# Performance work log

Hardware: AMD Instinct MI355X
Metric: run time of the kernel (lower is better)

The kernel has to match this reference:

```python
import jax, jax.numpy as jnp
import numpy as np

N_NODES = 100000
N_EDGES = 1600000
N_GRAPHS = 128
IN_CH, OUT_CH, N_CLASS = 768, 128, 2


def setup_inputs() -> dict:
    key = jax.random.key(0)
    ks = jax.random.split(key, 8)
    x = jax.random.normal(ks[0], (N_NODES, IN_CH), dtype=jnp.float32)
    # directed edges with src < dst so to_undirected (concat + reverse) has no duplicates
    src = jax.random.randint(ks[1], (N_EDGES,), 0, N_NODES - 1, dtype=jnp.int32)
    dst = jax.random.randint(ks[2], (N_EDGES,), 1, N_NODES, dtype=jnp.int32)
    dst = jnp.where(dst <= src, src + 1, dst)  # ensure src < dst (no self-loops)
    edge_index = jnp.stack([src, dst], axis=0)
    batch = jnp.sort(jax.random.randint(ks[3], (N_NODES,), 0, N_GRAPHS, dtype=jnp.int32))
    s = 0.05
    return {
        "x": x,
        "edge_index": edge_index,
        "batch": batch,
        "num_graphs": N_GRAPHS,
        "W_conv": jax.random.normal(ks[4], (IN_CH, OUT_CH), dtype=jnp.float32) * s,
        "b_conv": jnp.zeros((OUT_CH,), dtype=jnp.float32),
        "W_lin0": jax.random.normal(ks[5], (IN_CH, OUT_CH), dtype=jnp.float32) * s,
        "b_lin0": jnp.zeros((OUT_CH,), dtype=jnp.float32),
        "W_lin1": jax.random.normal(ks[6], (2 * OUT_CH, OUT_CH), dtype=jnp.float32) * s,
        "b_lin1": jnp.zeros((OUT_CH,), dtype=jnp.float32),
        "W_lin2": jax.random.normal(ks[7], (OUT_CH, N_CLASS), dtype=jnp.float32) * s,
        "b_lin2": jnp.zeros((N_CLASS,), dtype=jnp.float32),
    }


def _gcn_conv(x, W, b, src, dst, n_nodes):
    # GCNConv: linear transform, add self-loops, symmetric normalization, scatter-add
    loop = jnp.arange(n_nodes, dtype=src.dtype)
    s = jnp.concatenate([src, loop])
    d = jnp.concatenate([dst, loop])
    deg = jax.ops.segment_sum(jnp.ones_like(d, dtype=x.dtype), d, num_segments=n_nodes)
    dinv = jnp.where(deg > 0, jax.lax.rsqrt(deg), 0.0)
    norm = dinv[s] * dinv[d]  # [E']
    h = x @ W  # [N, out]
    msg = h[s] * norm[:, None]  # gather + scale
    return jax.ops.segment_sum(msg, d, num_segments=n_nodes) + b


def reference(x, edge_index, batch, num_graphs, W_conv, b_conv,
              W_lin0, b_lin0, W_lin1, b_lin1, W_lin2, b_lin2):
    n_nodes = x.shape[0]
    # to_undirected: add reversed edges (input has src<dst so no duplicates to coalesce)
    src = jnp.concatenate([edge_index[0], edge_index[1]])
    dst = jnp.concatenate([edge_index[1], edge_index[0]])
    h = jax.nn.relu(_gcn_conv(x, W_conv, b_conv, src, dst, n_nodes))
    # global max pool over graphs
    h = jax.ops.segment_max(h, batch, num_segments=num_graphs)  # [G, out]
    # root node = first node of each graph (batch is sorted)
    root = jax.ops.segment_min(jnp.arange(n_nodes), batch, num_segments=num_graphs)
    news = jax.nn.relu(x[root] @ W_lin0 + b_lin0)  # [G, out]
    h = jax.nn.relu(jnp.concatenate([news, h], axis=-1) @ W_lin1 + b_lin1)
    logits = h @ W_lin2 + b_lin2
    return jax.nn.log_softmax(logits, axis=-1)
```

## Files before the change

### kernel.cpp

```cpp
#include <hip/hip_runtime.h>

#define N_NODES 100000
#define N_EDGES 1600000
#define N_GRAPHS 128
#define IN_CH 768
#define OUT_CH 128

#define BSHIFT 8
#define NBKT ((N_NODES + 255) / 256)
#define EPB 8000
#define CAPREC 16384
#define PADV 16
#define CAPADJ (CAPREC + 256 * (PADV - 1))

using short8 = __attribute__((ext_vector_type(8))) short;
using f32x4  = __attribute__((ext_vector_type(4))) float;

__device__ __forceinline__ float bf2f(unsigned short u) {
    return __uint_as_float(((unsigned)u) << 16);
}
__device__ __forceinline__ unsigned short f2bf(float f) {
    unsigned u = __float_as_uint(f);
    u += 0x7fffu + ((u >> 16) & 1u);
    return (unsigned short)(u >> 16);
}
__device__ __forceinline__ float load_f(const void* p, size_t i, int f32) {
    return f32 ? ((const float*)p)[i] : bf2f(((const unsigned short*)p)[i]);
}
__device__ __forceinline__ float lo16(unsigned p) { return __uint_as_float(p << 16); }
__device__ __forceinline__ float hi16(unsigned p) { return __uint_as_float(p & 0xffff0000u); }

__global__ void k_init(int* flag, int* gcur, unsigned* pooled, int* root,
                       const int* __restrict__ batch, const unsigned short* __restrict__ xbits,
                       const void* Wc, const void* bc, const void* W0, const void* b0,
                       const void* W1, const void* b1, const void* W2, const void* b2,
                       unsigned short* Wt, float* fbc, float* fW0, float* fb0,
                       float* fW1, float* fb1, float* fW2, float* fb2) {
    __shared__ int sflag;
    if (threadIdx.x == 0) sflag = 0;
    __syncthreads();
    int bad = 0;
    for (int j = threadIdx.x; j < 8192; j += 256) {
        float v = bf2f(xbits[j]);
        if (!(v > -64.f && v < 64.f)) bad = 1;
    }
    if (bad) atomicOr(&sflag, 1);
    __syncthreads();
    int f32 = sflag;
    int i = blockIdx.x * blockDim.x + threadIdx.x;
    if (i == 0) *flag = f32;
    if (i < NBKT) gcur[i] = i * CAPREC;
    if (i < N_GRAPHS * OUT_CH) pooled[i] = 0u;
    if (i < N_NODES) {
        int b = batch[i];
        if (i == 0 || batch[i - 1] != b) root[b] = i;
    }
    if (i < IN_CH * OUT_CH) {
        int n = i / IN_CH, k = i - n * IN_CH;
        Wt[i] = f32 ? f2bf(((const float*)Wc)[k * OUT_CH + n])
                    : ((const unsigned short*)Wc)[k * OUT_CH + n];
        fW0[i] = load_f(W0, i, f32);
    }
    if (i < 2 * OUT_CH * OUT_CH) fW1[i] = load_f(W1, i, f32);
    if (i < OUT_CH * 2) fW2[i] = load_f(W2, i, f32);
    if (i < OUT_CH) { fbc[i] = load_f(bc, i, f32); fb0[i] = load_f(b0, i, f32); fb1[i] = load_f(b1, i, f32); }
    if (i < 2) fb2[i] = load_f(b2, i, f32);
}

__global__ __launch_bounds__(256) void k_bin(const int* __restrict__ src, const int* __restrict__ dst,
                                             int* gcur, unsigned* __restrict__ binned) {
    __shared__ int hist[NBKT];
    __shared__ int basep[NBKT];
    int t = threadIdx.x;
    for (int b = t; b < NBKT; b += 256) hist[b] = 0;
    __syncthreads();
    int e0 = blockIdx.x * EPB, e1 = e0 + EPB;
    if (e1 > N_EDGES) e1 = N_EDGES;
    for (int i = e0 + t; i < e1; i += 256) {
        unsigned s_ = (unsigned)src[i]; if (s_ >= N_NODES) s_ = N_NODES - 1u;
        unsigned d_ = (unsigned)dst[i]; if (d_ >= N_NODES) d_ = N_NODES - 1u;
        atomicAdd(&hist[d_ >> BSHIFT], 1);
        atomicAdd(&hist[s_ >> BSHIFT], 1);
    }
    __syncthreads();
    for (int b = t; b < NBKT; b += 256) {
        int c = hist[b];
        if (c) {
            int base = atomicAdd(&gcur[b], c);
            basep[b] = (base + c <= (b + 1) * CAPREC) ? base : -1;
        }
        hist[b] = 0;
    }
    __syncthreads();
    for (int i = e0 + t; i < e1; i += 256) {
        unsigned s_ = (unsigned)src[i]; if (s_ >= N_NODES) s_ = N_NODES - 1u;
        unsigned d_ = (unsigned)dst[i]; if (d_ >= N_NODES) d_ = N_NODES - 1u;
        unsigned bd = d_ >> BSHIFT, bs = s_ >> BSHIFT;
        int pd_ = basep[bd], ps_ = basep[bs];
        int od = atomicAdd(&hist[bd], 1);
        int os = atomicAdd(&hist[bs], 1);
        if (pd_ >= 0) binned[pd_ + od] = (s_ << 8) | (d_ & 255u);
        if (ps_ >= 0) binned[ps_ + os] = (d_ << 8) | (s_ & 255u);
    }
}

__global__ __launch_bounds__(256) void k_build(const unsigned* __restrict__ binned,
                                               const int* __restrict__ gcur,
                                               int2* odeg, float* dinv, int* adj) {
    __shared__ int sdeg[256], scur[256], sscan[256];
    int b = blockIdx.x, t = threadIdx.x;
    int base = b * CAPREC;
    int n = gcur[b] - base;
    if (n > CAPREC) n = CAPREC;
    if (n < 0) n = 0;
    int base_adj = b * CAPADJ;
    sdeg[t] = 0;
    __syncthreads();
    for (int j = t; j < n; j += 256) atomicAdd(&sdeg[binned[base + j] & 255u], 1);
    __syncthreads();
    int myd = sdeg[t];
    int pd = (myd + PADV - 1) & ~(PADV - 1);
    sscan[t] = pd;
    __syncthreads();
    for (int off = 1; off < 256; off <<= 1) {
        int add = (t >= off) ? sscan[t - off] : 0;
        __syncthreads();
        sscan[t] += add;
        __syncthreads();
    }
    int excl = sscan[t] - pd;
    int node = (b << BSHIFT) + t;
    if (node < N_NODES) {
        odeg[node] = make_int2(base_adj + excl, pd);
        dinv[node] = rsqrtf((float)(myd + 1));
    }
    for (int j = myd; j < pd; j++) adj[base_adj + excl + j] = N_NODES;
    scur[t] = excl;
    __syncthreads();
    for (int j = t; j < n; j += 256) {
        unsigned rec = binned[base + j];
        int loc = rec & 255u;
        adj[base_adj + atomicAdd(&scur[loc], 1)] = (int)(rec >> 8);
    }
}

#define MBLK 128
#define BK 64
#define LSTR 72

__global__ __launch_bounds__(256) void k_gemm(const int* __restrict__ flag,
                                              const void* __restrict__ xv,
                                              const unsigned short* __restrict__ Wt,
                                              const float* __restrict__ dinv,
                                              unsigned short* __restrict__ h) {
    __shared__ __align__(16) unsigned short As[MBLK * LSTR];
    __shared__ __align__(16) unsigned short Bs[OUT_CH * LSTR];
    const int f32 = *flag;
    const int tid = threadIdx.x;
    if (blockIdx.x == 0 && tid < 64) ((unsigned*)(h + (size_t)N_NODES * OUT_CH))[tid] = 0u;
    const int wave = tid >> 6, lane = tid & 63;
    const int quad = lane >> 4, l16 = lane & 15;
    const int wm = (wave >> 1) * 64, wn = (wave & 1) * 64;
    const int row0 = blockIdx.x * MBLK;

    f32x4 acc[4][4];
#pragma unroll
    for (int mt = 0; mt < 4; mt++)
#pragma unroll
        for (int nt = 0; nt < 4; nt++) acc[mt][nt] = (f32x4){0.f, 0.f, 0.f, 0.f};

    int r_[4], c8_[4];
    size_t arow_[4];
#pragma unroll
    for (int i = 0; i < 4; i++) {
        int chunk = tid + i * 256;
        r_[i] = chunk >> 3;
        c8_[i] = (chunk & 7) << 3;
        int gr = row0 + r_[i]; if (gr >= N_NODES) gr = N_NODES - 1;
        arow_[i] = (size_t)gr * IN_CH;
    }

    float4 fa[4][2];
    uint4  ua[4];
    uint4  rb[4];

#define LOADK(K0)                                                                      \
    {                                                                                  \
        if (f32) {                                                                     \
            _Pragma("unroll") for (int i = 0; i < 4; i++) {                            \
                const float* xp = (const float*)xv + arow_[i] + (K0) + c8_[i];         \
                fa[i][0] = *(const float4*)xp;                                         \
                fa[i][1] = *(const float4*)(xp + 4);                                   \
            }                                                                          \
        } else {                                                                       \
            _Pragma("unroll") for (int i = 0; i < 4; i++)                              \
                ua[i] = *(const uint4*)((const unsigned short*)xv + arow_[i] + (K0) + c8_[i]); \
        }                                                                              \
        _Pragma("unroll") for (int i = 0; i < 4; i++)                                  \
            rb[i] = *(const uint4*)(Wt + (size_t)r_[i] * IN_CH + (K0) + c8_[i]);       \
    }

#define STOREK()                                                                       \
    {                                                                                  \
        if (f32) {                                                                     \
            _Pragma("unroll") for (int i = 0; i < 4; i++) {                            \
                uint4 va;                                                              \
                va.x = (unsigned)f2bf(fa[i][0].x) | ((unsigned)f2bf(fa[i][0].y) << 16);\
                va.y = (unsigned)f2bf(fa[i][0].z) | ((unsigned)f2bf(fa[i][0].w) << 16);\
                va.z = (unsigned)f2bf(fa[i][1].x) | ((unsigned)f2bf(fa[i][1].y) << 16);\
                va.w = (unsigned)f2bf(fa[i][1].z) | ((unsigned)f2bf(fa[i][1].w) << 16);\
                *(uint4*)&As[r_[i] * LSTR + c8_[i]] = va;                              \
                *(uint4*)&Bs[r_[i] * LSTR + c8_[i]] = rb[i];                           \
            }                                                                          \
        } else {                                                                       \
            _Pragma("unroll") for (int i = 0; i < 4; i++) {                            \
                *(uint4*)&As[r_[i] * LSTR + c8_[i]] = ua[i];                           \
                *(uint4*)&Bs[r_[i] * LSTR + c8_[i]] = rb[i];                           \
            }                                                                          \
        }                                                                              \
    }

#define COMPUTE()                                                                      \
    {                                                                                  \
        _Pragma("unroll") for (int kk = 0; kk < BK; kk += 32) {                        \
            short8 af[4], bf[4];                                                       \
            _Pragma("unroll") for (int mt = 0; mt < 4; mt++)                           \
                af[mt] = *(const short8*)&As[(wm + mt * 16 + l16) * LSTR + kk + quad * 8]; \
            _Pragma("unroll") for (int nt = 0; nt < 4; nt++)                           \
                bf[nt] = *(const short8*)&Bs[(wn + nt * 16 + l16) * LSTR + kk + quad * 8]; \
            _Pragma("unroll") for (int mt = 0; mt < 4; mt++)                           \
                _Pragma("unroll") for (int nt = 0; nt < 4; nt++)                       \
                    acc[mt][nt] = __builtin_amdgcn_mfma_f32_16x16x32_bf16(af[mt], bf[nt], acc[mt][nt], 0, 0, 0); \
        }                                                                              \
    }

    LOADK(0);
    STOREK();
    __syncthreads();
    for (int k0 = BK;; k0 += BK) {
        bool more = (k0 < IN_CH);
        if (more) LOADK(k0);
        COMPUTE();
        if (!more) break;
        __syncthreads();
        STOREK();
        __syncthreads();
    }

#pragma unroll
    for (int mt = 0; mt < 4; mt++) {
#pragma unroll
        for (int r = 0; r < 4; r++) {
            int m = row0 + wm + mt * 16 + quad * 4 + r;
            if (m >= N_NODES) continue;
            float dvm = dinv[m];
#pragma unroll
            for (int nt = 0; nt < 4; nt++) {
                int col = wn + nt * 16 + l16;
                h[(size_t)m * OUT_CH + col] = f2bf(acc[mt][nt][r] * dvm);
            }
        }
    }
#undef LOADK
#undef STOREK
#undef COMPUTE
}

__global__ __launch_bounds__(256) void k_agg(const unsigned short* __restrict__ h,
                                             const int* __restrict__ adj,
                                             const int2* __restrict__ odeg,
                                             const float* __restrict__ dinv,
                                             const int* __restrict__ batch,
                                             const float* __restrict__ fbc,
                                             unsigned* pooled) {
    int wave = threadIdx.x >> 6, lane = threadIdx.x & 63;
    int node = blockIdx.x * 4 + wave;
    float dv = dinv[node];
    int l16 = lane & 15;

    uint4 own = *(const uint4*)(h + (size_t)node * OUT_CH + l16 * 8);
    float gsel = (lane < 16) ? 1.f : 0.f;
    float a0 = lo16(own.x) * gsel, a1 = hi16(own.x) * gsel;
    float a2 = lo16(own.y) * gsel, a3 = hi16(own.y) * gsel;
    float a4 = lo16(own.z) * gsel, a5 = hi16(own.z) * gsel;
    float a6 = lo16(own.w) * gsel, a7 = hi16(own.w) * gsel;

    int2 od = odeg[node];
    int o = od.x, e = od.x + od.y;
#define GATH(q)                                                              \
    {                                                                        \
        unsigned rlo = (lane & 16) ? (q).y : (q).x;                          \
        unsigned rhi = (lane & 16) ? (q).w : (q).z;                          \
        unsigned row = (lane & 32) ? rhi : rlo;                              \
        uint4 pv = *(const uint4*)(h + (size_t)row * OUT_CH + l16 * 8);      \
        a0 += lo16(pv.x); a1 += hi16(pv.x);                                  \
        a2 += lo16(pv.y); a3 += hi16(pv.y);                                  \
        a4 += lo16(pv.z); a5 += hi16(pv.z);                                  \
        a6 += lo16(pv.w); a7 += hi16(pv.w);                                  \
    }
    for (int i = o; i < e; i += 16) {
        uint4 q0 = *(const uint4*)&adj[i];
        uint4 q1 = *(const uint4*)&adj[i + 4];
        uint4 q2 = *(const uint4*)&adj[i + 8];
        uint4 q3 = *(const uint4*)&adj[i + 12];
        GATH(q0) GATH(q1) GATH(q2) GATH(q3)
    }
#undef GATH

    a0 += __shfl_xor(a0, 16, 64); a1 += __shfl_xor(a1, 16, 64);
    a2 += __shfl_xor(a2, 16, 64); a3 += __shfl_xor(a3, 16, 64);
    a4 += __shfl_xor(a4, 16, 64); a5 += __shfl_xor(a5, 16, 64);
    a6 += __shfl_xor(a6, 16, 64); a7 += __shfl_xor(a7, 16, 64);
    a0 += __shfl_xor(a0, 32, 64); a1 += __shfl_xor(a1, 32, 64);
    a2 += __shfl_xor(a2, 32, 64); a3 += __shfl_xor(a3, 32, 64);
    a4 += __shfl_xor(a4, 32, 64); a5 += __shfl_xor(a5, 32, 64);
    a6 += __shfl_xor(a6, 32, 64); a7 += __shfl_xor(a7, 32, 64);

    float4 bA = *(const float4*)&fbc[l16 * 8];
    float4 bB = *(const float4*)&fbc[l16 * 8 + 4];
    float r0 = fmaxf(fmaf(a0, dv, bA.x), 0.f);
    float r1 = fmaxf(fmaf(a1, dv, bA.y), 0.f);
    float r2 = fmaxf(fmaf(a2, dv, bA.z), 0.f);
    float r3 = fmaxf(fmaf(a3, dv, bA.w), 0.f);
    float r4 = fmaxf(fmaf(a4, dv, bB.x), 0.f);
    float r5 = fmaxf(fmaf(a5, dv, bB.y), 0.f);
    float r6 = fmaxf(fmaf(a6, dv, bB.z), 0.f);
    float r7 = fmaxf(fmaf(a7, dv, bB.w), 0.f);

    int g = batch[node];
    __shared__ float s0[256], s1[256];
    __shared__ int sg[4];
    if (lane < 16) {
        *(float4*)&s0[wave * 64 + l16 * 4] = (float4){r0, r2, r4, r6};
        *(float4*)&s1[wave * 64 + l16 * 4] = (float4){r1, r3, r5, r7};
        if (l16 == 0) sg[wave] = g;
    }
    __syncthreads();
    if (wave == 0) {
        int g0 = sg[0];
        if (sg[1] == g0 && sg[2] == g0 && sg[3] == g0) {
            float m0 = fmaxf(fmaxf(s0[lane], s0[64 + lane]), fmaxf(s0[128 + lane], s0[192 + lane]));
            float m1 = fmaxf(fmaxf(s1[lane], s1[64 + lane]), fmaxf(s1[128 + lane], s1[192 + lane]));
            atomicMax(&pooled[g0 * OUT_CH + lane * 2],     __float_as_uint(m0));
            atomicMax(&pooled[g0 * OUT_CH + lane * 2 + 1], __float_as_uint(m1));
        } else {
#pragma unroll
            for (int w = 0; w < 4; w++) {
                atomicMax(&pooled[sg[w] * OUT_CH + lane * 2],     __float_as_uint(s0[w * 64 + lane]));
                atomicMax(&pooled[sg[w] * OUT_CH + lane * 2 + 1], __float_as_uint(s1[w * 64 + lane]));
            }
        }
    }
}

__global__ __launch_bounds__(256) void k_final(const int* __restrict__ flag,
                                               const void* __restrict__ x,
                                               const int* __restrict__ root,
                                               const unsigned* __restrict__ pooled,
                                               const float* __restrict__ W0,
                                               const float* __restrict__ b0,
                                               const float* __restrict__ W1,
                                               const float* __restrict__ b1,
                                               const float* __restrict__ W2,
                                               const float* __restrict__ b2,
                                               void* out) {
    __shared__ float xs[IN_CH];
    __shared__ float ps[256];
    __shared__ float ins[2 * OUT_CH];
    __shared__ float h2s[OUT_CH];
    int f32 = *flag;
    int g = blockIdx.x, t = threadIdx.x;
    int r = root[g]; if ((unsigned)r >= N_NODES) r = 0;
    for (int j = t; j < IN_CH; j += 256) xs[j] = load_f(x, (size_t)r * IN_CH + j, f32);
    if (t >= 128) ins[OUT_CH + (t - 128)] = __uint_as_float(pooled[g * OUT_CH + (t - 128)]);
    __syncthreads();
    {
        int c = t & 127, half = t >> 7;
        int k0 = half * (IN_CH / 2);
        float acc = 0.f;
#pragma unroll 8
        for (int k = 0; k < IN_CH / 2; k++) acc += xs[k0 + k] * W0[(size_t)(k0 + k) * OUT_CH + c];
        ps[t] = acc;
    }
    __syncthreads();
    if (t < 128) ins[t] = fmaxf(ps[t] + ps[t + 128] + b0[t], 0.f);
    __syncthreads();
    {
        int c = t & 127, half = t >> 7;
        int k0 = half * OUT_CH;
        float acc = 0.f;
#pragma unroll 8
        for (int k = 0; k < OUT_CH; k++) acc += ins[k0 + k] * W1[(size_t)(k0 + k) * OUT_CH + c];
        ps[t] = acc;
    }
    __syncthreads();
    if (t < 128) h2s[t] = fmaxf(ps[t] + ps[t + 128] + b1[t], 0.f);
    __syncthreads();
    if (t == 0) {
        float l0 = b2[0], l1 = b2[1];
        for (int k = 0; k < OUT_CH; k++) { float v = h2s[k]; l0 += v * W2[k * 2]; l1 += v * W2[k * 2 + 1]; }
        float m = fmaxf(l0, l1);
        float ls = m + logf(expf(l0 - m) + expf(l1 - m));
        if (f32) {
            ((float*)out)[g * 2]     = l0 - ls;
            ((float*)out)[g * 2 + 1] = l1 - ls;
        } else {
            ((unsigned short*)out)[g * 2]     = f2bf(l0 - ls);
            ((unsigned short*)out)[g * 2 + 1] = f2bf(l1 - ls);
        }
    }
}

extern "C" void kernel_launch(void* const* d_in, const int* in_sizes, int n_in,
                              void* d_out, int out_size, void* d_ws, size_t ws_size,
                              hipStream_t stream) {
    const void* x     = d_in[0];
    const int*  ei    = (const int*)d_in[1];
    const int*  batch = (const int*)d_in[2];
    const void* Wc    = d_in[4];
    const void* bc    = d_in[5];
    const void* W0    = d_in[6];
    const void* b0    = d_in[7];
    const void* W1    = d_in[8];
    const void* b1    = d_in[9];
    const void* W2    = d_in[10];
    const void* b2    = d_in[11];
    const int* src = ei;
    const int* dst = ei + N_EDGES;

    char* p = (char*)d_ws;
    auto carve = [&](size_t bytes) -> void* {
        void* r = (void*)p;
        p += (bytes + 255) & ~(size_t)255;
        return r;
    };
    int*      flag      = (int*)carve(4);
    int*      gcur      = (int*)carve((size_t)NBKT * 4);
    int2*     odeg      = (int2*)carve((size_t)N_NODES * 8);
    float*    dinv      = (float*)carve((size_t)N_NODES * 4);
    int*      root      = (int*)carve(128 * 4);
    unsigned* pooled    = (unsigned*)carve((size_t)N_GRAPHS * OUT_CH * 4);
    unsigned short* Wt  = (unsigned short*)carve((size_t)IN_CH * OUT_CH * 2);
    float*    fW0       = (float*)carve((size_t)IN_CH * OUT_CH * 4);
    float*    fW1       = (float*)carve((size_t)2 * OUT_CH * OUT_CH * 4);
    float*    fW2       = (float*)carve((size_t)OUT_CH * 2 * 4);
    float*    fbc       = (float*)carve((size_t)OUT_CH * 4);
    float*    fb0       = (float*)carve((size_t)OUT_CH * 4);
    float*    fb1       = (float*)carve((size_t)OUT_CH * 4);
    float*    fb2       = (float*)carve(2 * 4);
    int*      adj       = (int*)carve((size_t)NBKT * CAPADJ * 4);
    size_t binned_bytes = (size_t)NBKT * CAPREC * 4;
    size_t h_bytes      = (size_t)(N_NODES + 1) * OUT_CH * 2;
    void*     hb        = carve(binned_bytes > h_bytes ? binned_bytes : h_bytes);
    unsigned* binned    = (unsigned*)hb;
    unsigned short* h   = (unsigned short*)hb;

    const int nEdgeBlk = (N_EDGES + EPB - 1) / EPB;

    k_init  <<<391, 256, 0, stream>>>(flag, gcur, pooled, root, batch, (const unsigned short*)x,
                                      Wc, bc, W0, b0, W1, b1, W2, b2,
                                      Wt, fbc, fW0, fb0, fW1, fb1, fW2, fb2);
    k_bin   <<<nEdgeBlk, 256, 0, stream>>>(src, dst, gcur, binned);
    k_build <<<NBKT, 256, 0, stream>>>(binned, gcur, odeg, dinv, adj);
    k_gemm  <<<(N_NODES + MBLK - 1) / MBLK, 256, 0, stream>>>(flag, x, Wt, dinv, h);
    k_agg   <<<N_NODES / 4, 256, 0, stream>>>(h, adj, odeg, dinv, batch, fbc, pooled);
    k_final <<<N_GRAPHS, 256, 0, stream>>>(flag, x, root, pooled, fW0, fb0, fW1, fb1, fW2, fb2, d_out);
}
```

Before: 697.5 us.

## Tune binning chunk, vectorize build loops, prefetch GEMM tiles, unroll gather

Several independent tweaks land together. The edges-per-block constant for binning drops from 8000 to 2000, which launches more blocks. The build kernel now reads binned records in pairs with uint2 loads. The GEMM main loop issues the global load for the tile after next right after the shared-memory store, so the load overlaps the following compute. The aggregation gather loop is unrolled to 32 neighbors per iteration to keep more loads in flight. These add register pressure and, in the binning kernel, more atomic contention across blocks.

```diff
diff --git a/kernel.cpp b/kernel.cpp
--- a/kernel.cpp
+++ b/kernel.cpp
@@ -8,7 +8,7 @@
 
 #define BSHIFT 8
 #define NBKT ((N_NODES + 255) / 256)
-#define EPB 8000
+#define EPB 2000
 #define CAPREC 16384
 #define PADV 16
 #define CAPADJ (CAPREC + 256 * (PADV - 1))
@@ -116,7 +116,13 @@
     int base_adj = b * CAPADJ;
     sdeg[t] = 0;
     __syncthreads();
-    for (int j = t; j < n; j += 256) atomicAdd(&sdeg[binned[base + j] & 255u], 1);
+    int npair = n & ~1;
+    for (int j = t * 2; j < npair; j += 512) {
+        uint2 rr = *(const uint2*)&binned[base + j];
+        atomicAdd(&sdeg[rr.x & 255u], 1);
+        atomicAdd(&sdeg[rr.y & 255u], 1);
+    }
+    if ((n & 1) && t == 0) atomicAdd(&sdeg[binned[base + n - 1] & 255u], 1);
     __syncthreads();
     int myd = sdeg[t];
     int pd = (myd + PADV - 1) & ~(PADV - 1);
@@ -137,10 +143,14 @@
     for (int j = myd; j < pd; j++) adj[base_adj + excl + j] = N_NODES;
     scur[t] = excl;
     __syncthreads();
-    for (int j = t; j < n; j += 256) {
-        unsigned rec = binned[base + j];
-        int loc = rec & 255u;
-        adj[base_adj + atomicAdd(&scur[loc], 1)] = (int)(rec >> 8);
+    for (int j = t * 2; j < npair; j += 512) {
+        uint2 rr = *(const uint2*)&binned[base + j];
+        adj[base_adj + atomicAdd(&scur[rr.x & 255u], 1)] = (int)(rr.x >> 8);
+        adj[base_adj + atomicAdd(&scur[rr.y & 255u], 1)] = (int)(rr.y >> 8);
+    }
+    if ((n & 1) && t == 0) {
+        unsigned rec = binned[base + n - 1];
+        adj[base_adj + atomicAdd(&scur[rec & 255u], 1)] = (int)(rec >> 8);
     }
 }
 
@@ -237,13 +247,14 @@
     LOADK(0);
     STOREK();
     __syncthreads();
-    for (int k0 = BK;; k0 += BK) {
-        bool more = (k0 < IN_CH);
-        if (more) LOADK(k0);
+    LOADK(BK);
+    for (int k0 = 0;; k0 += BK) {
         COMPUTE();
-        if (!more) break;
+        int kn = k0 + BK;
+        if (kn >= IN_CH) break;
         __syncthreads();
         STOREK();
+        if (kn + BK < IN_CH) LOADK(kn + BK);
         __syncthreads();
     }
 
@@ -298,7 +309,20 @@
         a4 += lo16(pv.z); a5 += hi16(pv.z);                                  \
         a6 += lo16(pv.w); a7 += hi16(pv.w);                                  \
     }
-    for (int i = o; i < e; i += 16) {
+    int i = o;
+    for (; i + 32 <= e; i += 32) {
+        uint4 q0 = *(const uint4*)&adj[i];
+        uint4 q1 = *(const uint4*)&adj[i + 4];
+        uint4 q2 = *(const uint4*)&adj[i + 8];
+        uint4 q3 = *(const uint4*)&adj[i + 12];
+        uint4 q4 = *(const uint4*)&adj[i + 16];
+        uint4 q5 = *(const uint4*)&adj[i + 20];
+        uint4 q6 = *(const uint4*)&adj[i + 24];
+        uint4 q7 = *(const uint4*)&adj[i + 28];
+        GATH(q0) GATH(q1) GATH(q2) GATH(q3)
+        GATH(q4) GATH(q5) GATH(q6) GATH(q7)
+    }
+    for (; i < e; i += 16) {
         uint4 q0 = *(const uint4*)&adj[i];
         uint4 q1 = *(const uint4*)&adj[i + 4];
         uint4 q2 = *(const uint4*)&adj[i + 8];
```

Measured after the change: 690.3 us (median of 2 runs). About the same (-1.0%).
